# Performance work log

Measured on AMD Instinct MI355X. Metric: run time of the kernel, lower is better.

Reference implementation:

```python
import jax, jax.numpy as jnp
import numpy as np

EPS = 1e-5

def layer_norm(x, w, b):
    mu = jnp.mean(x, axis=-1, keepdims=True)
    var = jnp.mean(jnp.square(x - mu), axis=-1, keepdims=True)
    return (x - mu) * jax.lax.rsqrt(var + EPS) * w + b

def setup_inputs() -> dict:
    key = jax.random.key(0)
    ks = jax.random.split(key, 16)
    B, N, c_z, c_h = 1, 512, 128, 128
    s_z = 1.0 / np.sqrt(c_z)
    s_h = 1.0 / np.sqrt(c_h)
    return {
        "z": jax.random.normal(ks[0], (B, N, N, c_z), jnp.float32),
        "mask": jnp.ones((B, N, N), jnp.float32),
        "norm_in_w": jnp.ones((c_z,), jnp.float32),
        "norm_in_b": jnp.zeros((c_z,), jnp.float32),
        "a_p_w": jax.random.normal(ks[1], (c_h, c_z), jnp.float32) * s_z,
        "a_p_b": jnp.zeros((c_h,), jnp.float32),
        "a_g_w": jax.random.normal(ks[2], (c_h, c_z), jnp.float32) * s_z,
        "a_g_b": jnp.ones((c_h,), jnp.float32),
        "b_p_w": jax.random.normal(ks[3], (c_h, c_z), jnp.float32) * s_z,
        "b_p_b": jnp.zeros((c_h,), jnp.float32),
        "b_g_w": jax.random.normal(ks[4], (c_h, c_z), jnp.float32) * s_z,
        "b_g_b": jnp.ones((c_h,), jnp.float32),
        "g_w": jax.random.normal(ks[5], (c_z, c_z), jnp.float32) * s_z,
        "g_b": jnp.ones((c_z,), jnp.float32),
        "z_w": jax.random.normal(ks[6], (c_z, c_h), jnp.float32) * s_h,
        "z_b": jnp.zeros((c_z,), jnp.float32),
        "norm_out_w": jnp.ones((c_h,), jnp.float32),
        "norm_out_b": jnp.zeros((c_h,), jnp.float32),
    }

OUTGOING = True

def reference(z, mask, norm_in_w, norm_in_b, a_p_w, a_p_b, a_g_w, a_g_b,
              b_p_w, b_p_b, b_g_w, b_g_b, g_w, g_b, z_w, z_b,
              norm_out_w, norm_out_b):
    # z: [B, N, N, c_z]; mask: [B, N, N]
    m = mask[..., None]  # [B, N, N, 1]
    zn = layer_norm(z, norm_in_w, norm_in_b)
    # gated projections (nn.Linear layout: W is [out, in])
    a = m * jax.nn.sigmoid(zn @ a_g_w.T + a_g_b) * (zn @ a_p_w.T + a_p_b)
    b = m * jax.nn.sigmoid(zn @ b_g_w.T + b_g_b) * (zn @ b_p_w.T + b_p_b)
    if OUTGOING:
        # x[i,j,c] = sum_k a[i,k,c] * b[j,k,c]
        x = jnp.einsum('bikc,bjkc->bijc', a, b)
    else:
        x = jnp.einsum('bkic,bkjc->bijc', a, b)
    x = layer_norm(x, norm_out_w, norm_out_b)
    x = x @ z_w.T + z_b
    g = jax.nn.sigmoid(zn @ g_w.T + g_b)
    return x * g
```

## Files before the change

### kernel.cpp

```cpp
#include <hip/hip_runtime.h>
#include <stddef.h>

#define NN 512
#define CC 128
#define NPOS (NN*NN)

typedef unsigned short u16;
typedef unsigned int   u32;
typedef u16  u16x4  __attribute__((ext_vector_type(4)));
typedef u16  u16x8  __attribute__((ext_vector_type(8)));
typedef __bf16 bf16x8 __attribute__((ext_vector_type(8)));
typedef float f32x4  __attribute__((ext_vector_type(4)));

__device__ __forceinline__ float b2f(u16 u) {
    union { u32 i; float f; } w; w.i = ((u32)u) << 16; return w.f;
}
__device__ __forceinline__ u16 f2b(float f) {
    return __builtin_bit_cast(u16, (__bf16)f);
}
__device__ __forceinline__ float sigm(float x) { return 1.0f / (1.0f + __expf(-x)); }

__device__ __forceinline__ void gld16(const u16* g, u16* l) {
    __builtin_amdgcn_global_load_lds(
        (const __attribute__((address_space(1))) u32*)g,
        (__attribute__((address_space(3))) u32*)l, 16, 0, 0);
}

struct W6 { const float* p[6]; };

__global__ __launch_bounds__(256) void k0_pack(W6 w, u16* __restrict__ dst)
{
    const int i = blockIdx.x * 256 + threadIdx.x;
    const int mt = i >> 14, r = i & 16383;
    const int cb = r >> 11, ks = (r >> 9) & 3, lane = (r >> 3) & 63, j = r & 7;
    const int row = cb * 16 + (lane & 15);
    const int col = ks * 32 + (lane >> 4) * 8 + j;
    dst[i] = f2b(w.p[mt][row * 128 + col]);
}

__global__ __launch_bounds__(128) void k1_ln_proj(
    const float* __restrict__ z,  const float* __restrict__ mask,
    const float* __restrict__ wi, const float* __restrict__ bi,
    const u16* __restrict__ wpk,
    const float* __restrict__ agb, const float* __restrict__ apb,
    const float* __restrict__ bgb, const float* __restrict__ bpb,
    u16* __restrict__ a_cm, u16* __restrict__ b_cm)
{
    __shared__ u16 zn[64][136];
    const int tid = threadIdx.x;
    const size_t p0 = (size_t)blockIdx.x * 64;

    {
        const float* zt = z + p0 * CC;
        const int g  = tid >> 5;
        const int c4 = (tid & 31) * 4;
        const f32x4 wi4 = *(const f32x4*)(wi + c4);
        const f32x4 bi4 = *(const f32x4*)(bi + c4);
        f32x4 v[16];
        #pragma unroll
        for (int h = 0; h < 16; ++h)
            v[h] = *(const f32x4*)(zt + h * 512 + tid * 4);
        #pragma unroll
        for (int h = 0; h < 16; ++h) {
            float s  = (v[h][0] + v[h][1]) + (v[h][2] + v[h][3]);
            float s2 = (v[h][0]*v[h][0] + v[h][1]*v[h][1])
                     + (v[h][2]*v[h][2] + v[h][3]*v[h][3]);
            #pragma unroll
            for (int ms = 1; ms <= 16; ms <<= 1) {
                s  += __shfl_xor(s,  ms);
                s2 += __shfl_xor(s2, ms);
            }
            const float mu   = s * (1.0f / CC);
            const float rstd = rsqrtf(s2 * (1.0f / CC) - mu * mu + 1e-5f);
            u16x4 o4;
            #pragma unroll
            for (int e = 0; e < 4; ++e) {
                const float nw = rstd * wi4[e];
                o4[e] = f2b(v[h][e] * nw + __builtin_fmaf(-mu, nw, bi4[e]));
            }
            *(u16x4*)&zn[h * 4 + g][c4] = o4;
        }
    }
    __syncthreads();

    const int wave = tid >> 6, lane = tid & 63;
    const int m = lane & 15, q = lane >> 4;

    bf16x8 af[2][4];
    #pragma unroll
    for (int t = 0; t < 2; ++t)
        #pragma unroll
        for (int ks = 0; ks < 4; ++ks)
            af[t][ks] = *(const bf16x8*)&zn[wave * 32 + t * 16 + m][ks * 32 + q * 8];

    f32x4 mkv[2];
    #pragma unroll
    for (int t = 0; t < 2; ++t)
        mkv[t] = *(const f32x4*)(mask + p0 + wave * 32 + t * 16 + q * 4);

    const float* Bv[4] = { agb, apb, bgb, bpb };

    for (int cb = 0; cb < 8; ++cb) {
        const int o = cb * 16 + m;
        f32x4 res[4][2];
        #pragma unroll
        for (int mt = 0; mt < 4; ++mt) {
            const float bvv = Bv[mt][o];
            #pragma unroll
            for (int t = 0; t < 2; ++t) res[mt][t] = f32x4{ bvv, bvv, bvv, bvv };
            const u16* wp = wpk + ((size_t)((mt * 8 + cb) * 4)) * 512 + (size_t)lane * 8;
            bf16x8 wf[4];
            #pragma unroll
            for (int ks = 0; ks < 4; ++ks) wf[ks] = *(const bf16x8*)(wp + ks * 512);
            #pragma unroll
            for (int ks = 0; ks < 4; ++ks)
                #pragma unroll
                for (int t = 0; t < 2; ++t)
                    res[mt][t] = __builtin_amdgcn_mfma_f32_16x16x32_bf16(
                                   af[t][ks], wf[ks], res[mt][t], 0, 0, 0);
        }
        #pragma unroll
        for (int t = 0; t < 2; ++t) {
            u16x4 av, bv;
            #pragma unroll
            for (int r = 0; r < 4; ++r) {
                const float mk = mkv[t][r];
                av[r] = f2b(mk * sigm(res[0][t][r]) * res[1][t][r]);
                bv[r] = f2b(mk * sigm(res[2][t][r]) * res[3][t][r]);
            }
            const size_t off = (size_t)o * NPOS + p0 + wave * 32 + t * 16 + q * 4;
            *(u16x4*)(a_cm + off) = av;
            *(u16x4*)(b_cm + off) = bv;
        }
    }
}

__global__ __launch_bounds__(256) void k2_gemm(
    const u16* __restrict__ A, const u16* __restrict__ B, u16* __restrict__ X)
{
    __shared__ u16 As[2][128][32];
    __shared__ u16 Bs[2][128][32];
    const int tid = threadIdx.x;
    const int bx  = blockIdx.x;
    const int c   = bx >> 4;
    const int i0  = ((bx >> 2) & 3) * 128;
    const int j0  = (bx & 3) * 128;
    const size_t cbase = (size_t)c * NPOS;
    const u16* Ac = A + cbase;
    const u16* Bc = B + cbase;

    const int wave = tid >> 6, lane = tid & 63;
    const int wm = wave >> 1, wn = wave & 1;
    const int m = lane & 15, q = lane >> 4;

    f32x4 acc[4][4];
    const f32x4 zero = { 0.f, 0.f, 0.f, 0.f };
    #pragma unroll
    for (int mt = 0; mt < 4; ++mt)
        #pragma unroll
        for (int nt = 0; nt < 4; ++nt) acc[mt][nt] = zero;

    for (int kt = 0; kt < 8; ++kt) {
        __syncthreads();
        #pragma unroll
        for (int ps = 0; ps < 4; ++ps) {
            const int id   = ps * 256 + tid;
            const int half = id >> 9;
            const int rw   = (id >> 2) & 127;
            const int g    = (id & 3) ^ ((rw >> 1) & 3);
            const size_t goff = (size_t)(kt * 64 + half * 32 + g * 8);
            gld16(Ac + (size_t)(i0 + rw) * NN + goff, &As[0][0][0] + id * 8);
            gld16(Bc + (size_t)(j0 + rw) * NN + goff, &Bs[0][0][0] + id * 8);
        }
        __syncthreads();
        #pragma unroll
        for (int ks = 0; ks < 2; ++ks) {
            bf16x8 af[4], bf[4];
            #pragma unroll
            for (int mt = 0; mt < 4; ++mt) {
                const int row = wm * 64 + mt * 16 + m;
                const int slot = q ^ ((row >> 1) & 3);
                af[mt] = *(const bf16x8*)&As[ks][row][slot * 8];
            }
            #pragma unroll
            for (int nt = 0; nt < 4; ++nt) {
                const int row = wn * 64 + nt * 16 + m;
                const int slot = q ^ ((row >> 1) & 3);
                bf[nt] = *(const bf16x8*)&Bs[ks][row][slot * 8];
            }
            #pragma unroll
            for (int mt = 0; mt < 4; ++mt)
                #pragma unroll
                for (int nt = 0; nt < 4; ++nt)
                    acc[mt][nt] = __builtin_amdgcn_mfma_f32_16x16x32_bf16(
                                    af[mt], bf[nt], acc[mt][nt], 0, 0, 0);
        }
    }

    #pragma unroll
    for (int mt = 0; mt < 4; ++mt) {
        #pragma unroll
        for (int r = 0; r < 4; ++r) {
            const int i = i0 + wm * 64 + mt * 16 + q * 4 + r;
            #pragma unroll
            for (int nt = 0; nt < 4; ++nt) {
                const int j = j0 + wn * 64 + nt * 16 + m;
                X[cbase + (size_t)i * NN + j] = f2b(acc[mt][nt][r]);
            }
        }
    }
}

__global__ __launch_bounds__(256) void k3_out(
    float* __restrict__ out, const u16* __restrict__ x_cm,
    const float* __restrict__ z,
    const float* __restrict__ wi, const float* __restrict__ bi,
    const float* __restrict__ wo, const float* __restrict__ bo,
    const u16* __restrict__ wpk,
    const float* __restrict__ gbv, const float* __restrict__ zbv)
{
    __shared__ u16 A[128][136];
    __shared__ u16 Bt[128][136];
    const int tid = threadIdx.x;
    const size_t p0 = (size_t)blockIdx.x * 128;
    const int wave = tid >> 6, lane = tid & 63;
    const int m = lane & 15, q = lane >> 4;
    const int pl = tid >> 1, ht = tid & 1;

    {
        const float* zr = z + (p0 + pl) * CC + ht * 64;
        float v[64];
        #pragma unroll
        for (int h = 0; h < 16; ++h) {
            f32x4 t = *(const f32x4*)(zr + h * 4);
            #pragma unroll
            for (int e = 0; e < 4; ++e) v[h * 4 + e] = t[e];
        }
        float s = 0.f, s2 = 0.f;
        #pragma unroll
        for (int e = 0; e < 64; ++e) { s += v[e]; s2 += v[e] * v[e]; }
        s  += __shfl_xor(s, 1);
        s2 += __shfl_xor(s2, 1);
        const float mu   = s * (1.0f / CC);
        const float rstd = rsqrtf(s2 * (1.0f / CC) - mu * mu + 1e-5f);
        #pragma unroll
        for (int h = 0; h < 8; ++h) {
            u16x8 o8;
            #pragma unroll
            for (int e = 0; e < 8; ++e) {
                const int c = ht * 64 + h * 8 + e;
                o8[e] = f2b((v[h * 8 + e] - mu) * rstd * wi[c] + bi[c]);
            }
            *(u16x8*)&A[pl][ht * 64 + h * 8] = o8;
        }
    }
    {
        const int c = tid >> 1, seg = tid & 1;
        #pragma unroll
        for (int e = 0; e < 8; ++e) {
            u16x8 vv = *(const u16x8*)(x_cm + (size_t)c * NPOS + p0 + seg * 64 + e * 8);
            *(u16x8*)&Bt[c][seg * 64 + e * 8] = vv;
        }
    }
    __syncthreads();

    bf16x8 afz[2][4];
    #pragma unroll
    for (int t = 0; t < 2; ++t)
        #pragma unroll
        for (int ks = 0; ks < 4; ++ks)
            afz[t][ks] = *(const bf16x8*)&A[wave * 32 + t * 16 + m][ks * 32 + q * 8];
    __syncthreads();

    {
        float v[64];
        #pragma unroll
        for (int e = 0; e < 64; ++e) v[e] = b2f(Bt[ht * 64 + e][pl]);
        float s = 0.f, s2 = 0.f;
        #pragma unroll
        for (int e = 0; e < 64; ++e) { s += v[e]; s2 += v[e] * v[e]; }
        s  += __shfl_xor(s, 1);
        s2 += __shfl_xor(s2, 1);
        const float mu   = s * (1.0f / CC);
        const float rstd = rsqrtf(s2 * (1.0f / CC) - mu * mu + 1e-5f);
        #pragma unroll
        for (int h = 0; h < 8; ++h) {
            u16x8 o8;
            #pragma unroll
            for (int e = 0; e < 8; ++e) {
                const int c = ht * 64 + h * 8 + e;
                o8[e] = f2b((v[h * 8 + e] - mu) * rstd * wo[c] + bo[c]);
            }
            *(u16x8*)&A[pl][ht * 64 + h * 8] = o8;
        }
    }
    __syncthreads();

    bf16x8 afx[2][4];
    #pragma unroll
    for (int t = 0; t < 2; ++t)
        #pragma unroll
        for (int ks = 0; ks < 4; ++ks)
            afx[t][ks] = *(const bf16x8*)&A[wave * 32 + t * 16 + m][ks * 32 + q * 8];

    for (int cb = 0; cb < 8; ++cb) {
        const int o = cb * 16 + m;
        const float gb0 = gbv[o], zb0 = zbv[o];
        f32x4 accg[2], accx[2];
        #pragma unroll
        for (int t = 0; t < 2; ++t) {
            accg[t] = f32x4{ gb0, gb0, gb0, gb0 };
            accx[t] = f32x4{ zb0, zb0, zb0, zb0 };
        }
        const u16* wpg = wpk + ((size_t)((4 * 8 + cb) * 4)) * 512 + (size_t)lane * 8;
        const u16* wpz = wpk + ((size_t)((5 * 8 + cb) * 4)) * 512 + (size_t)lane * 8;
        bf16x8 wg[4], wz[4];
        #pragma unroll
        for (int ks = 0; ks < 4; ++ks) {
            wg[ks] = *(const bf16x8*)(wpg + ks * 512);
            wz[ks] = *(const bf16x8*)(wpz + ks * 512);
        }
        #pragma unroll
        for (int ks = 0; ks < 4; ++ks)
            #pragma unroll
            for (int t = 0; t < 2; ++t) {
                accg[t] = __builtin_amdgcn_mfma_f32_16x16x32_bf16(
                            afz[t][ks], wg[ks], accg[t], 0, 0, 0);
                accx[t] = __builtin_amdgcn_mfma_f32_16x16x32_bf16(
                            afx[t][ks], wz[ks], accx[t], 0, 0, 0);
            }
        #pragma unroll
        for (int t = 0; t < 2; ++t)
            #pragma unroll
            for (int r = 0; r < 4; ++r) {
                const size_t p = p0 + wave * 32 + t * 16 + q * 4 + r;
                out[p * CC + o] = accx[t][r] * sigm(accg[t][r]);
            }
    }
}

extern "C" void kernel_launch(void* const* d_in, const int* in_sizes, int n_in,
                              void* d_out, int out_size, void* d_ws, size_t ws_size,
                              hipStream_t stream)
{
    const float* z    = (const float*)d_in[0];
    const float* mask = (const float*)d_in[1];
    const float* wi   = (const float*)d_in[2];
    const float* bi   = (const float*)d_in[3];
    const float* apw  = (const float*)d_in[4];
    const float* apb  = (const float*)d_in[5];
    const float* agw  = (const float*)d_in[6];
    const float* agb  = (const float*)d_in[7];
    const float* bpw  = (const float*)d_in[8];
    const float* bpb  = (const float*)d_in[9];
    const float* bgw  = (const float*)d_in[10];
    const float* bgb  = (const float*)d_in[11];
    const float* gw   = (const float*)d_in[12];
    const float* gb   = (const float*)d_in[13];
    const float* zw   = (const float*)d_in[14];
    const float* zb   = (const float*)d_in[15];
    const float* wo   = (const float*)d_in[16];
    const float* bo   = (const float*)d_in[17];

    u16* a_cm = (u16*)d_ws;
    u16* b_cm = a_cm + (size_t)CC * NPOS;
    u16* x_cm = b_cm + (size_t)CC * NPOS;
    u16* w_pk = x_cm + (size_t)CC * NPOS;
    float* out = (float*)d_out;

    W6 w6; w6.p[0] = agw; w6.p[1] = apw; w6.p[2] = bgw; w6.p[3] = bpw;
    w6.p[4] = gw; w6.p[5] = zw;

    k0_pack<<<6 * 16384 / 256, 256, 0, stream>>>(w6, w_pk);
    k1_ln_proj<<<NPOS / 64, 128, 0, stream>>>(z, mask, wi, bi, w_pk,
                                              agb, apb, bgb, bpb, a_cm, b_cm);
    k2_gemm<<<128 * 16, 256, 0, stream>>>(a_cm, b_cm, x_cm);
    k3_out<<<NPOS / 128, 256, 0, stream>>>(out, x_cm, z, wi, bi, wo, bo,
                                           w_pk, gb, zb);
}
```

Baseline: 493.2 us.

## Stage k1 projection outputs in swizzled LDS for coalesced channel-major stores

The LN+projection kernel now processes 128 positions per 256-thread block and writes the gated a/b results into an XOR-swizzled shared-memory tile. It then emits 16-byte, contiguous per-channel stores instead of scattered 8-byte writes. Biases and mask are hoisted into registers up front, and the LN staging buffer reuses the same swizzled LDS. The cost is 64KB of LDS per block, which reduces occupancy, plus extra syncs.

After: 509.6 us. 3.3% more time.

```diff
diff --git a/kernel.cpp b/kernel.cpp
--- a/kernel.cpp
+++ b/kernel.cpp
@@ -38,7 +38,7 @@
     dst[i] = f2b(w.p[mt][row * 128 + col]);
 }
 
-__global__ __launch_bounds__(128) void k1_ln_proj(
+__global__ __launch_bounds__(256) void k1_ln_proj(
     const float* __restrict__ z,  const float* __restrict__ mask,
     const float* __restrict__ wi, const float* __restrict__ bi,
     const u16* __restrict__ wpk,
@@ -46,9 +46,26 @@
     const float* __restrict__ bgb, const float* __restrict__ bpb,
     u16* __restrict__ a_cm, u16* __restrict__ b_cm)
 {
-    __shared__ u16 zn[64][136];
+    __shared__ u16 res[2][128][128];
     const int tid = threadIdx.x;
-    const size_t p0 = (size_t)blockIdx.x * 64;
+    const size_t p0 = (size_t)blockIdx.x * 128;
+
+    const int wave = tid >> 6, lane = tid & 63;
+    const int m = lane & 15, q = lane >> 4;
+
+    float bias[4][8];
+    {
+        const float* Bv[4] = { agb, apb, bgb, bpb };
+        #pragma unroll
+        for (int mt = 0; mt < 4; ++mt)
+            #pragma unroll
+            for (int cb = 0; cb < 8; ++cb)
+                bias[mt][cb] = Bv[mt][cb * 16 + m];
+    }
+    f32x4 mkv[2];
+    #pragma unroll
+    for (int t = 0; t < 2; ++t)
+        mkv[t] = *(const f32x4*)(mask + p0 + wave * 32 + t * 16 + q * 4);
 
     {
         const float* zt = z + p0 * CC;
@@ -59,7 +76,7 @@
         f32x4 v[16];
         #pragma unroll
         for (int h = 0; h < 16; ++h)
-            v[h] = *(const f32x4*)(zt + h * 512 + tid * 4);
+            v[h] = *(const f32x4*)(zt + h * 1024 + tid * 4);
         #pragma unroll
         for (int h = 0; h < 16; ++h) {
             float s  = (v[h][0] + v[h][1]) + (v[h][2] + v[h][3]);
@@ -78,36 +95,31 @@
                 const float nw = rstd * wi4[e];
                 o4[e] = f2b(v[h][e] * nw + __builtin_fmaf(-mu, nw, bi4[e]));
             }
-            *(u16x4*)&zn[h * 4 + g][c4] = o4;
-        }
-    }
-    __syncthreads();
-
-    const int wave = tid >> 6, lane = tid & 63;
-    const int m = lane & 15, q = lane >> 4;
+            *(u16x4*)((char*)&res[0][h * 8 + g][0] + ((c4 * 2) ^ (g << 4))) = o4;
+        }
+    }
+    __syncthreads();
 
     bf16x8 af[2][4];
     #pragma unroll
     for (int t = 0; t < 2; ++t)
         #pragma unroll
-        for (int ks = 0; ks < 4; ++ks)
-            af[t][ks] = *(const bf16x8*)&zn[wave * 32 + t * 16 + m][ks * 32 + q * 8];
-
-    f32x4 mkv[2];
-    #pragma unroll
-    for (int t = 0; t < 2; ++t)
-        mkv[t] = *(const f32x4*)(mask + p0 + wave * 32 + t * 16 + q * 4);
-
-    const float* Bv[4] = { agb, apb, bgb, bpb };
-
+        for (int ks = 0; ks < 4; ++ks) {
+            const int row = wave * 32 + t * 16 + m;
+            af[t][ks] = *(const bf16x8*)((const char*)&res[0][row][0]
+                          + (((ks * 32 + q * 8) * 2) ^ ((m & 7) << 4)));
+        }
+    __syncthreads();
+
+    #pragma unroll 2
     for (int cb = 0; cb < 8; ++cb) {
         const int o = cb * 16 + m;
-        f32x4 res[4][2];
+        f32x4 racc[4][2];
         #pragma unroll
         for (int mt = 0; mt < 4; ++mt) {
-            const float bvv = Bv[mt][o];
-            #pragma unroll
-            for (int t = 0; t < 2; ++t) res[mt][t] = f32x4{ bvv, bvv, bvv, bvv };
+            const float bvv = bias[mt][cb];
+            #pragma unroll
+            for (int t = 0; t < 2; ++t) racc[mt][t] = f32x4{ bvv, bvv, bvv, bvv };
             const u16* wp = wpk + ((size_t)((mt * 8 + cb) * 4)) * 512 + (size_t)lane * 8;
             bf16x8 wf[4];
             #pragma unroll
@@ -116,8 +128,8 @@
             for (int ks = 0; ks < 4; ++ks)
                 #pragma unroll
                 for (int t = 0; t < 2; ++t)
-                    res[mt][t] = __builtin_amdgcn_mfma_f32_16x16x32_bf16(
-                                   af[t][ks], wf[ks], res[mt][t], 0, 0, 0);
+                    racc[mt][t] = __builtin_amdgcn_mfma_f32_16x16x32_bf16(
+                                   af[t][ks], wf[ks], racc[mt][t], 0, 0, 0);
         }
         #pragma unroll
         for (int t = 0; t < 2; ++t) {
@@ -125,12 +137,29 @@
             #pragma unroll
             for (int r = 0; r < 4; ++r) {
                 const float mk = mkv[t][r];
-                av[r] = f2b(mk * sigm(res[0][t][r]) * res[1][t][r]);
-                bv[r] = f2b(mk * sigm(res[2][t][r]) * res[3][t][r]);
-            }
-            const size_t off = (size_t)o * NPOS + p0 + wave * 32 + t * 16 + q * 4;
-            *(u16x4*)(a_cm + off) = av;
-            *(u16x4*)(b_cm + off) = bv;
+                av[r] = f2b(mk * sigm(racc[0][t][r]) * racc[1][t][r]);
+                bv[r] = f2b(mk * sigm(racc[2][t][r]) * racc[3][t][r]);
+            }
+            const int pw2 = (wave * 32 + t * 16 + q * 4) * 2;
+            const int sw  = pw2 ^ ((o & 7) << 4);
+            *(u16x4*)((char*)&res[0][o][0] + sw) = av;
+            *(u16x4*)((char*)&res[1][o][0] + sw) = bv;
+        }
+    }
+    __syncthreads();
+
+    #pragma unroll
+    for (int it = 0; it < 2; ++it) {
+        const int task = it * 256 + tid;
+        const int arr  = task >> 8;
+        const int ch   = (task >> 1) & 127;
+        const int seg  = task & 1;
+        u16* dst = (arr ? b_cm : a_cm) + (size_t)ch * NPOS + p0 + seg * 64;
+        const char* src = (const char*)&res[arr][ch][0];
+        #pragma unroll
+        for (int e = 0; e < 8; ++e) {
+            *(u16x8*)(dst + e * 8) =
+                *(const u16x8*)(src + (((seg * 128 + e * 16)) ^ ((ch & 7) << 4)));
         }
     }
 }
@@ -372,8 +401,8 @@
     w6.p[4] = gw; w6.p[5] = zw;
 
     k0_pack<<<6 * 16384 / 256, 256, 0, stream>>>(w6, w_pk);
-    k1_ln_proj<<<NPOS / 64, 128, 0, stream>>>(z, mask, wi, bi, w_pk,
-                                              agb, apb, bgb, bpb, a_cm, b_cm);
+    k1_ln_proj<<<NPOS / 128, 256, 0, stream>>>(z, mask, wi, bi, w_pk,
+                                               agb, apb, bgb, bpb, a_cm, b_cm);
     k2_gemm<<<128 * 16, 256, 0, stream>>>(a_cm, b_cm, x_cm);
     k3_out<<<NPOS / 128, 256, 0, stream>>>(out, x_cm, z, wi, bi, wo, bo,
                                            w_pk, gb, zb);
```
